# Performance work log

Measured on AMD Instinct MI355X. Metric: run time of the kernel, lower is better.

The kernel has to match this reference:

```python
import jax, jax.numpy as jnp
import numpy as np

NUM_HEADS = 16
ROPE_BASE = 10000.0


def _rope_cos_sin(seq_len, head_dim, dtype):
    inv_freq = 1.0 / (ROPE_BASE ** (jnp.arange(0, head_dim, 2, dtype=jnp.float32) / head_dim))
    t = jnp.arange(seq_len, dtype=jnp.float32)
    freqs = jnp.einsum('i,j->ij', t, inv_freq)            # [S, hd/2]
    emb = jnp.concatenate((freqs, freqs), axis=-1)         # [S, hd]
    return emb.astype(dtype).cos if False else (jnp.cos(emb).astype(dtype), jnp.sin(emb).astype(dtype))


def _rotate_half(x):
    x1, x2 = jnp.split(x, 2, axis=-1)
    return jnp.concatenate((-x2, x1), axis=-1)


def setup_inputs() -> dict:
    key = jax.random.key(0)
    ks = jax.random.split(key, 5)
    B, S, D = 2, 2048, 2048
    x = jax.random.normal(ks[0], (B, S, D), dtype=jnp.float32)
    sc = 1.0 / np.sqrt(D)
    Wq = jax.random.normal(ks[1], (D, D), dtype=jnp.float32) * sc
    Wk = jax.random.normal(ks[2], (D, D), dtype=jnp.float32) * sc
    Wv = jax.random.normal(ks[3], (D, D), dtype=jnp.float32) * sc
    Wo = jax.random.normal(ks[4], (D, D), dtype=jnp.float32) * sc
    mask = jnp.tril(jnp.ones((S, S), dtype=bool))[None, None]  # causal [1,1,S,S]
    return {"x": x, "Wq": Wq, "Wk": Wk, "Wv": Wv, "Wo": Wo, "mask": mask}


def reference(x, Wq, Wk, Wv, Wo, mask):
    B, S, D = x.shape
    H = NUM_HEADS
    hd = D // H
    scale = hd ** -0.5

    def split_heads(t):
        return t.reshape(B, S, H, hd).transpose(0, 2, 1, 3)  # [B,H,S,hd]

    q = split_heads(x @ Wq.T)
    k = split_heads(x @ Wk.T)
    v = split_heads(x @ Wv.T)

    cos, sin = _rope_cos_sin(S, hd, x.dtype)                 # [S,hd]
    cos = cos[None, None]
    sin = sin[None, None]
    q = q * cos + _rotate_half(q) * sin
    k = k * cos + _rotate_half(k) * sin

    scores = jnp.einsum('bhqd,bhkd->bhqk', q, k) * scale
    scores = jnp.where(mask, scores, jnp.finfo(scores.dtype).min)
    attn = jax.nn.softmax(scores, axis=-1)                    # dropout p applied in eval mode -> identity
    out = jnp.einsum('bhqk,bhkd->bhqd', attn, v)
    out = out.transpose(0, 2, 1, 3).reshape(B, S, D)
    return out @ Wo.T
```

## Files before the change

kernel.cpp:

```cpp
#include <hip/hip_runtime.h>
#include <math.h>

#define S_LEN 2048
#define D_MODEL 2048
#define NHEADS 16
#define HDIM 128
#define BATCH 2
#define MTOT (BATCH * S_LEN)

typedef unsigned short u16;
typedef __attribute__((ext_vector_type(8))) short short8;
typedef __attribute__((ext_vector_type(4))) float floatx4;
typedef __attribute__((ext_vector_type(4))) float float4v;

__device__ __forceinline__ u16 f2bf(float f) {
    union { float f; unsigned u; } v; v.f = f;
    unsigned r = v.u + 0x7fff + ((v.u >> 16) & 1);
    return (u16)(r >> 16);
}
__device__ __forceinline__ float bf2f(u16 b) {
    union { unsigned u; float f; } v; v.u = ((unsigned)b) << 16;
    return v.f;
}

__device__ __forceinline__ void gl_lds16(const void* g, void* l) {
    __builtin_amdgcn_global_load_lds(
        (const __attribute__((address_space(1))) unsigned int*)g,
        (__attribute__((address_space(3))) unsigned int*)l, 16, 0, 0);
}

__device__ __forceinline__ int swzA(int row, int col) {
    return row * 128 + (((col >> 3) ^ (row & 7)) << 3) + (col & 7);
}
__device__ __forceinline__ int swzB(int row, int col) {
    return row * 64 + (((col >> 3) ^ (row & 7)) << 3) + (col & 7);
}

__global__ void convert_in(const float* __restrict__ src, u16* __restrict__ dst) {
    int t = blockIdx.x * blockDim.x + threadIdx.x;
    float4v a = ((const float4v*)src)[t * 2];
    float4v b = ((const float4v*)src)[t * 2 + 1];
    union { short8 v; u16 e[8]; } o;
    o.e[0] = f2bf(a[0]); o.e[1] = f2bf(a[1]); o.e[2] = f2bf(a[2]); o.e[3] = f2bf(a[3]);
    o.e[4] = f2bf(b[0]); o.e[5] = f2bf(b[1]); o.e[6] = f2bf(b[2]); o.e[7] = f2bf(b[3]);
    *(short8*)(dst + (size_t)t * 8) = o.v;
}

__global__ __launch_bounds__(256, 2) void gemm_nt(const u16* __restrict__ A,
                                                  const u16* __restrict__ W,
                                                  u16* __restrict__ Cb,
                                                  float* __restrict__ Cf,
                                                  int K) {
    __shared__ __align__(16) u16 lA[128 * 64];
    __shared__ __align__(16) u16 lB[128 * 64];
    const int tid = threadIdx.x;
    const int wave = tid >> 6, lane = tid & 63;
    const int l15 = lane & 15, quad = lane >> 4;
    const int mtile = blockIdx.y * 128;
    const int ntile = blockIdx.x * 128;
    const int wm = (wave >> 1) * 64, wn = (wave & 1) * 64;

    floatx4 acc[4][4] = {};

    for (int k0 = 0; k0 < K; k0 += 64) {
        __syncthreads();
#pragma unroll
        for (int i = 0; i < 4; ++i) {
            int slot = i * 256 + tid;
            int row = slot >> 3, kc = slot & 7;
            gl_lds16(A + (size_t)(mtile + row) * K + k0 + kc * 8,
                     &lA[(size_t)(i * 256 + wave * 64) * 8]);
            gl_lds16(W + (size_t)(ntile + row) * K + k0 + kc * 8,
                     &lB[(size_t)(i * 256 + wave * 64) * 8]);
        }
        __syncthreads();
#pragma unroll
        for (int ks = 0; ks < 2; ++ks) {
            short8 af[4], bf[4];
#pragma unroll
            for (int rf = 0; rf < 4; ++rf)
                af[rf] = *(const short8*)&lA[(wm + rf * 16 + l15) * 64 + ks * 32 + quad * 8];
#pragma unroll
            for (int cf = 0; cf < 4; ++cf)
                bf[cf] = *(const short8*)&lB[(wn + cf * 16 + l15) * 64 + ks * 32 + quad * 8];
#pragma unroll
            for (int rf = 0; rf < 4; ++rf)
#pragma unroll
                for (int cf = 0; cf < 4; ++cf)
                    acc[rf][cf] = __builtin_amdgcn_mfma_f32_16x16x32_bf16(
                        af[rf], bf[cf], acc[rf][cf], 0, 0, 0);
        }
    }
#pragma unroll
    for (int rf = 0; rf < 4; ++rf)
#pragma unroll
        for (int cf = 0; cf < 4; ++cf)
#pragma unroll
            for (int r = 0; r < 4; ++r) {
                size_t row = mtile + wm + rf * 16 + quad * 4 + r;
                size_t col = ntile + wn + cf * 16 + l15;
                if (Cb) Cb[row * D_MODEL + col] = f2bf(acc[rf][cf][r]);
                else    Cf[row * D_MODEL + col] = acc[rf][cf][r];
            }
}

__global__ void rope_kernel(u16* __restrict__ Q, u16* __restrict__ Kb) {
    int idx = blockIdx.x * blockDim.x + threadIdx.x;
    int jg = idx & 7;
    int h = (idx >> 3) & 15;
    int token = idx >> 7;
    int s = token & (S_LEN - 1);
    size_t base = (size_t)token * D_MODEL + h * HDIM + jg * 8;
    union { short8 v; u16 e[8]; } q1, q2, k1, k2, oq1, oq2, ok1, ok2;
    q1.v = *(const short8*)(Q + base);  q2.v = *(const short8*)(Q + base + 64);
    k1.v = *(const short8*)(Kb + base); k2.v = *(const short8*)(Kb + base + 64);
#pragma unroll
    for (int e = 0; e < 8; ++e) {
        int j = jg * 8 + e;
        float invf = exp2f(-(float)j * 0.20762050593046995f);
        float ang = (float)s * invf;
        float c = cosf(ang), sn = sinf(ang);
        float a = bf2f(q1.e[e]), b = bf2f(q2.e[e]);
        oq1.e[e] = f2bf(a * c - b * sn);
        oq2.e[e] = f2bf(b * c + a * sn);
        float ka = bf2f(k1.e[e]), kb2 = bf2f(k2.e[e]);
        ok1.e[e] = f2bf(ka * c - kb2 * sn);
        ok2.e[e] = f2bf(kb2 * c + ka * sn);
    }
    *(short8*)(Q + base) = oq1.v;  *(short8*)(Q + base + 64) = oq2.v;
    *(short8*)(Kb + base) = ok1.v; *(short8*)(Kb + base + 64) = ok2.v;
}

__global__ void transpose_v(const u16* __restrict__ V, u16* __restrict__ Vt) {
    __shared__ u16 t[64][66];
    int b = blockIdx.z;
    int s0 = blockIdx.x * 64;
    int c0 = blockIdx.y * 64;
    int tid = threadIdx.x;
#pragma unroll
    for (int i = 0; i < 2; ++i) {
        int slot = i * 256 + tid;
        int r = slot >> 3, cc = slot & 7;
        union { short8 v; u16 a[8]; } u;
        u.v = *(const short8*)(V + (size_t)(b * S_LEN + s0 + r) * D_MODEL + c0 + cc * 8);
#pragma unroll
        for (int e = 0; e < 8; ++e) t[r][cc * 8 + e] = u.a[e];
    }
    __syncthreads();
#pragma unroll
    for (int i = 0; i < 2; ++i) {
        int slot = i * 256 + tid;
        int d = slot >> 3, sc = slot & 7;
        union { short8 v; u16 a[8]; } o;
#pragma unroll
        for (int e = 0; e < 8; ++e) o.a[e] = t[sc * 8 + e][d];
        int col = c0 + d;
        int h = col >> 7, dd = col & 127;
        u16* dst = Vt + ((size_t)((b * NHEADS + h) * HDIM + dd)) * S_LEN + s0 + sc * 8;
        *(short8*)dst = o.v;
    }
}

__global__ __launch_bounds__(256, 2) void flash_attn(const u16* __restrict__ Q,
                                                     const u16* __restrict__ Kb,
                                                     const u16* __restrict__ Vt,
                                                     u16* __restrict__ O) {
    __shared__ __align__(16) u16 lK0[64 * 128];
    __shared__ __align__(16) u16 lK1[64 * 128];
    __shared__ __align__(16) u16 lV0[128 * 64];
    __shared__ __align__(16) u16 lV1[128 * 64];
    __shared__ __align__(16) u16 lP[4 * 32 * 64];
    const int bid = blockIdx.x;
    const int qt = bid & 15;
    const int bh = bid >> 4;
    const int h = bh & 15;
    const int b = bh >> 4;
    const int tid = threadIdx.x;
    const int wave = tid >> 6, lane = tid & 63;
    const int l15 = lane & 15, quad = lane >> 4;
    const int qbase = qt * 128;
    const int wrow = wave * 32;

    short8 qf[2][4];
#pragma unroll
    for (int rf = 0; rf < 2; ++rf)
#pragma unroll
        for (int ks = 0; ks < 4; ++ks)
            qf[rf][ks] = *(const short8*)(Q +
                (size_t)(b * S_LEN + qbase + wrow + rf * 16 + l15) * D_MODEL +
                h * HDIM + ks * 32 + quad * 8);

    floatx4 oacc[2][8] = {};
    float mrow[2][4], lrow[2][4];
#pragma unroll
    for (int rf = 0; rf < 2; ++rf)
#pragma unroll
        for (int r = 0; r < 4; ++r) { mrow[rf][r] = -1e30f; lrow[rf][r] = 0.f; }

    const float scale = 0.08838834764831845f;
    const int NT = 2 * (qt + 1);

#define STAGE_K(dK, kb_)                                                        \
    {                                                                           \
        _Pragma("unroll")                                                       \
        for (int i = 0; i < 4; ++i) {                                           \
            int slot = i * 256 + tid;                                           \
            int krow = slot >> 4, ksc = slot & 15;                              \
            int kssc = ksc ^ (krow & 7);                                        \
            gl_lds16(Kb + (size_t)(b * S_LEN + (kb_) + krow) * D_MODEL +        \
                         h * HDIM + kssc * 8,                                   \
                     (dK) + (size_t)(i * 256 + wave * 64) * 8);                 \
        }                                                                       \
    }
#define STAGE_V(dV, kb_)                                                        \
    {                                                                           \
        _Pragma("unroll")                                                       \
        for (int i = 0; i < 4; ++i) {                                           \
            int slot = i * 256 + tid;                                           \
            int vro = slot >> 3, vsc = slot & 7;                                \
            int vssc = vsc ^ (vro & 7);                                         \
            gl_lds16(Vt + ((size_t)(bh * HDIM + vro)) * S_LEN + (kb_) +         \
                         vssc * 8,                                              \
                     (dV) + (size_t)(i * 256 + wave * 64) * 8);                 \
        }                                                                       \
    }

    STAGE_K(lK0, 0);
    STAGE_V(lV0, 0);
    asm volatile("s_waitcnt vmcnt(0)" ::: "memory");
    u16* pbuf = lP + (size_t)wave * 32 * 64;

    for (int kt2 = 0; kt2 < NT; ++kt2) {
        u16* cK = (kt2 & 1) ? lK1 : lK0;
        u16* cV = (kt2 & 1) ? lV1 : lV0;
        u16* nK = (kt2 & 1) ? lK0 : lK1;
        u16* nV = (kt2 & 1) ? lV0 : lV1;
        const int kbase = kt2 * 64;
        const bool last = (kt2 + 1 == NT);

        __builtin_amdgcn_sched_barrier(0);
        __builtin_amdgcn_s_barrier();
        __builtin_amdgcn_sched_barrier(0);

        floatx4 sacc[2][4] = {};
#pragma unroll
        for (int ks = 0; ks < 4; ++ks) {
            short8 kf[4];
#pragma unroll
            for (int cf = 0; cf < 4; ++cf)
                kf[cf] = *(const short8*)&cK[swzA(cf * 16 + l15, ks * 32 + quad * 8)];
#pragma unroll
            for (int rf = 0; rf < 2; ++rf)
#pragma unroll
                for (int cf = 0; cf < 4; ++cf)
                    sacc[rf][cf] = __builtin_amdgcn_mfma_f32_16x16x32_bf16(
                        qf[rf][ks], kf[cf], sacc[rf][cf], 0, 0, 0);
        }

        if (!last) {
            STAGE_K(nK, kbase + 64);
            STAGE_V(nV, kbase + 64);
        }

        const bool diag = (kt2 >= 2 * qt);
        const int coff = kbase - qbase;
#pragma unroll
        for (int rf = 0; rf < 2; ++rf) {
#pragma unroll
            for (int r = 0; r < 4; ++r) {
                const int qrow = wrow + rf * 16 + quad * 4 + r;
                float vmax = -1e30f;
#pragma unroll
                for (int cf = 0; cf < 4; ++cf) {
                    float sv = sacc[rf][cf][r] * scale;
                    if (diag && (coff + cf * 16 + l15) > qrow) sv = -1e30f;
                    sacc[rf][cf][r] = sv;
                    vmax = fmaxf(vmax, sv);
                }
#pragma unroll
                for (int m = 8; m >= 1; m >>= 1)
                    vmax = fmaxf(vmax, __shfl_xor(vmax, m, 16));
                float mnew = fmaxf(mrow[rf][r], vmax);
                float alpha = __expf(mrow[rf][r] - mnew);
                mrow[rf][r] = mnew;
                float rsum = 0.f;
#pragma unroll
                for (int cf = 0; cf < 4; ++cf) {
                    float p = __expf(sacc[rf][cf][r] - mnew);
                    sacc[rf][cf][r] = p;
                    rsum += p;
                }
#pragma unroll
                for (int m = 8; m >= 1; m >>= 1) rsum += __shfl_xor(rsum, m, 16);
                lrow[rf][r] = lrow[rf][r] * alpha + rsum;
#pragma unroll
                for (int cf = 0; cf < 8; ++cf) oacc[rf][cf][r] *= alpha;
            }
        }

#pragma unroll
        for (int rf = 0; rf < 2; ++rf)
#pragma unroll
            for (int cf = 0; cf < 4; ++cf)
#pragma unroll
                for (int r = 0; r < 4; ++r)
                    pbuf[swzB(rf * 16 + quad * 4 + r, cf * 16 + l15)] =
                        f2bf(sacc[rf][cf][r]);

        asm volatile("s_waitcnt lgkmcnt(0)" ::: "memory");
        __builtin_amdgcn_sched_barrier(0);

#pragma unroll
        for (int ks2 = 0; ks2 < 2; ++ks2) {
            short8 pf[2], vf[8];
#pragma unroll
            for (int rf = 0; rf < 2; ++rf)
                pf[rf] = *(const short8*)&pbuf[swzB(rf * 16 + l15, ks2 * 32 + quad * 8)];
#pragma unroll
            for (int cf = 0; cf < 8; ++cf)
                vf[cf] = *(const short8*)&cV[swzB(cf * 16 + l15, ks2 * 32 + quad * 8)];
#pragma unroll
            for (int rf = 0; rf < 2; ++rf)
#pragma unroll
                for (int cf = 0; cf < 8; ++cf)
                    oacc[rf][cf] = __builtin_amdgcn_mfma_f32_16x16x32_bf16(
                        pf[rf], vf[cf], oacc[rf][cf], 0, 0, 0);
        }

        asm volatile("s_waitcnt vmcnt(0)" ::: "memory");
        __builtin_amdgcn_sched_barrier(0);
    }
#undef STAGE_K
#undef STAGE_V

#pragma unroll
    for (int rf = 0; rf < 2; ++rf)
#pragma unroll
        for (int r = 0; r < 4; ++r) {
            float inv = 1.0f / lrow[rf][r];
            int row = qbase + wrow + rf * 16 + quad * 4 + r;
#pragma unroll
            for (int cf = 0; cf < 8; ++cf) {
                int col = h * HDIM + cf * 16 + l15;
                O[(size_t)(b * S_LEN + row) * D_MODEL + col] = f2bf(oacc[rf][cf][r] * inv);
            }
        }
}

extern "C" void kernel_launch(void* const* d_in, const int* in_sizes, int n_in,
                              void* d_out, int out_size, void* d_ws, size_t ws_size,
                              hipStream_t stream) {
    const float* x  = (const float*)d_in[0];
    const float* Wq = (const float*)d_in[1];
    const float* Wk = (const float*)d_in[2];
    const float* Wv = (const float*)d_in[3];
    const float* Wo = (const float*)d_in[4];
    float* out = (float*)d_out;

    const size_t NX = (size_t)MTOT * D_MODEL;
    const size_t NW = (size_t)D_MODEL * D_MODEL;
    u16* base = (u16*)d_ws;
    u16* Qb  = base;
    u16* Kb  = base + NX;
    u16* Vb  = base + 2 * NX;
    u16* xb  = base + 3 * NX;
    u16* Vt  = xb;
    u16* Hb  = base + 4 * NX;
    u16* wqb = Kb;
    u16* wkb = Vb;
    u16* Ob  = Qb;

    dim3 blk(256);
    hipLaunchKernelGGL(convert_in, dim3(NX / 2048), blk, 0, stream, x,  xb);
    hipLaunchKernelGGL(convert_in, dim3(NW / 2048), blk, 0, stream, Wq, wqb);
    hipLaunchKernelGGL(convert_in, dim3(NW / 2048), blk, 0, stream, Wk, wkb);
    hipLaunchKernelGGL(convert_in, dim3(NW / 2048), blk, 0, stream, Wv, Hb);

    dim3 gg(D_MODEL / 128, MTOT / 128);
    hipLaunchKernelGGL(gemm_nt, gg, blk, 0, stream, xb, wqb, Qb, (float*)nullptr, D_MODEL);
    hipLaunchKernelGGL(gemm_nt, gg, blk, 0, stream, xb, wkb, Kb, (float*)nullptr, D_MODEL);
    hipLaunchKernelGGL(gemm_nt, gg, blk, 0, stream, xb, Hb,  Vb, (float*)nullptr, D_MODEL);
    hipLaunchKernelGGL(convert_in, dim3(NW / 2048), blk, 0, stream, Wo, Hb);
    hipLaunchKernelGGL(rope_kernel, dim3((MTOT * NHEADS * 8) / 256), blk, 0, stream, Qb, Kb);
    hipLaunchKernelGGL(transpose_v, dim3(S_LEN / 64, D_MODEL / 64, BATCH), blk, 0, stream, Vb, Vt);
    hipLaunchKernelGGL(flash_attn, dim3(BATCH * NHEADS * (S_LEN / 128)), blk, 0, stream,
                       Qb, Kb, Vt, Ob);
    hipLaunchKernelGGL(gemm_nt, gg, blk, 0, stream, Ob, Hb, (u16*)nullptr, out, D_MODEL);
}
```

Baseline: 506.5 us.

## Double-buffer LDS tiles in projection GEMM to overlap global loads with MFMA

The projection GEMM now uses two LDS buffers for A and W, so the direct global-to-LDS loads for the next K tile are issued between the two MFMA half-steps of the current tile. This is meant to hide global load latency behind compute and removes one block barrier per iteration. LDS use per block doubles to 64 KB, which may limit the two-blocks-per-CU occupancy target. It also relies on a vmcnt wait plus a single barrier per iteration being enough ordering.

Result: faster. 488.2 us (-3.6%).

```diff
diff --git a/kernel.cpp b/kernel.cpp
--- a/kernel.cpp
+++ b/kernel.cpp
@@ -51,8 +51,10 @@
                                                   u16* __restrict__ Cb,
                                                   float* __restrict__ Cf,
                                                   int K) {
-    __shared__ __align__(16) u16 lA[128 * 64];
-    __shared__ __align__(16) u16 lB[128 * 64];
+    __shared__ __align__(16) u16 lA0[128 * 64];
+    __shared__ __align__(16) u16 lA1[128 * 64];
+    __shared__ __align__(16) u16 lB0[128 * 64];
+    __shared__ __align__(16) u16 lB1[128 * 64];
     const int tid = threadIdx.x;
     const int wave = tid >> 6, lane = tid & 63;
     const int l15 = lane & 15, quad = lane >> 4;
@@ -61,28 +63,42 @@
     const int wm = (wave >> 1) * 64, wn = (wave & 1) * 64;
 
     floatx4 acc[4][4] = {};
-
-    for (int k0 = 0; k0 < K; k0 += 64) {
-        __syncthreads();
-#pragma unroll
-        for (int i = 0; i < 4; ++i) {
-            int slot = i * 256 + tid;
-            int row = slot >> 3, kc = slot & 7;
-            gl_lds16(A + (size_t)(mtile + row) * K + k0 + kc * 8,
-                     &lA[(size_t)(i * 256 + wave * 64) * 8]);
-            gl_lds16(W + (size_t)(ntile + row) * K + k0 + kc * 8,
-                     &lB[(size_t)(i * 256 + wave * 64) * 8]);
-        }
-        __syncthreads();
-#pragma unroll
-        for (int ks = 0; ks < 2; ++ks) {
+    const int NT = K >> 6;
+
+#define GSTAGE(dA, dB, k0_)                                                     \
+    {                                                                           \
+        _Pragma("unroll")                                                       \
+        for (int i = 0; i < 4; ++i) {                                           \
+            int slot = i * 256 + tid;                   \
+            int row = slot >> 3, kc = slot & 7;                                 \
+            gl_lds16(A + (size_t)(mtile + row) * K + (k0_) + kc * 8,            \
+                     (dA) + (size_t)(i * 256 + wave * 64) * 8);                 \
+            gl_lds16(W + (size_t)(ntile + row) * K + (k0_) + kc * 8,            \
+                     (dB) + (size_t)(i * 256 + wave * 64) * 8);                 \
+        }                                                                       \
+    }
+
+    GSTAGE(lA0, lB0, 0);
+    asm volatile("s_waitcnt vmcnt(0)" ::: "memory");
+
+    for (int t = 0; t < NT; ++t) {
+        u16* cA = (t & 1) ? lA1 : lA0;
+        u16* cB = (t & 1) ? lB1 : lB0;
+        u16* nA = (t & 1) ? lA0 : lA1;
+        u16* nB = (t & 1) ? lB0 : lB1;
+
+        __builtin_amdgcn_sched_barrier(0);
+        __builtin_amdgcn_s_barrier();
+        __builtin_amdgcn_sched_barrier(0);
+
+        {
             short8 af[4], bf[4];
 #pragma unroll
             for (int rf = 0; rf < 4; ++rf)
-                af[rf] = *(const short8*)&lA[(wm + rf * 16 + l15) * 64 + ks * 32 + quad * 8];
+                af[rf] = *(const short8*)&cA[(wm + rf * 16 + l15) * 64 + quad * 8];
 #pragma unroll
             for (int cf = 0; cf < 4; ++cf)
-                bf[cf] = *(const short8*)&lB[(wn + cf * 16 + l15) * 64 + ks * 32 + quad * 8];
+                bf[cf] = *(const short8*)&cB[(wn + cf * 16 + l15) * 64 + quad * 8];
 #pragma unroll
             for (int rf = 0; rf < 4; ++rf)
 #pragma unroll
@@ -90,7 +106,30 @@
                     acc[rf][cf] = __builtin_amdgcn_mfma_f32_16x16x32_bf16(
                         af[rf], bf[cf], acc[rf][cf], 0, 0, 0);
         }
-    }
+
+        if (t + 1 < NT) GSTAGE(nA, nB, (t + 1) * 64);
+
+        {
+            short8 af[4], bf[4];
+#pragma unroll
+            for (int rf = 0; rf < 4; ++rf)
+                af[rf] = *(const short8*)&cA[(wm + rf * 16 + l15) * 64 + 32 + quad * 8];
+#pragma unroll
+            for (int cf = 0; cf < 4; ++cf)
+                bf[cf] = *(const short8*)&cB[(wn + cf * 16 + l15) * 64 + 32 + quad * 8];
+#pragma unroll
+            for (int rf = 0; rf < 4; ++rf)
+#pragma unroll
+                for (int cf = 0; cf < 4; ++cf)
+                    acc[rf][cf] = __builtin_amdgcn_mfma_f32_16x16x32_bf16(
+                        af[rf], bf[cf], acc[rf][cf], 0, 0, 0);
+        }
+
+        asm volatile("s_waitcnt vmcnt(0)" ::: "memory");
+        __builtin_amdgcn_sched_barrier(0);
+    }
+#undef GSTAGE
+
 #pragma unroll
     for (int rf = 0; rf < 4; ++rf)
 #pragma unroll
```
